# Performance work log

Measured on AMD Instinct MI355X. Metric: run time of the kernel, lower is better.

Reference implementation:

```python
import jax, jax.numpy as jnp
import numpy as np

N = 100000      # nodes
E = 1600000     # edges (before self-loops)
F_IN = 512      # input features
H = 8           # heads layer 1
D = 8           # per-head dim layer 1
C = 40          # classes (layer 2 out, heads=1)
NEG_SLOPE = 0.2 # PyG GATConv default negative_slope


def setup_inputs() -> dict:
    key = jax.random.key(0)
    ks = jax.random.split(key, 10)
    x = jax.random.normal(ks[0], (N, F_IN), jnp.float32)
    edge_index = jax.random.randint(ks[1], (2, E), 0, N, dtype=jnp.int32)
    W1 = jax.random.normal(ks[2], (F_IN, H * D), jnp.float32) / np.float32(np.sqrt(F_IN))
    att_src1 = jax.random.normal(ks[3], (H, D), jnp.float32) / np.float32(np.sqrt(D))
    att_dst1 = jax.random.normal(ks[4], (H, D), jnp.float32) / np.float32(np.sqrt(D))
    b1 = jnp.zeros((H * D,), jnp.float32)
    W2 = jax.random.normal(ks[5], (H * D, C), jnp.float32) / np.float32(np.sqrt(H * D))
    att_src2 = jax.random.normal(ks[6], (1, C), jnp.float32) / np.float32(np.sqrt(C))
    att_dst2 = jax.random.normal(ks[7], (1, C), jnp.float32) / np.float32(np.sqrt(C))
    b2 = jnp.zeros((C,), jnp.float32)
    return {"x": x, "edge_index": edge_index, "W1": W1, "att_src1": att_src1,
            "att_dst1": att_dst1, "b1": b1, "W2": W2, "att_src2": att_src2,
            "att_dst2": att_dst2, "b2": b2}


def _gat_layer(x, src, dst, W, a_src, a_dst, heads, dim):
    # Dense projection, then per-head attention logits.
    h = (x @ W).reshape(-1, heads, dim)            # [N, H, D]
    alpha_s = jnp.einsum('nhd,hd->nh', h, a_src)   # [N, H]
    alpha_d = jnp.einsum('nhd,hd->nh', h, a_dst)
    e = jax.nn.leaky_relu(alpha_s[src] + alpha_d[dst], NEG_SLOPE)  # [E, H]
    # Segment softmax over edges grouped by destination node.
    emax = jax.ops.segment_max(e, dst, num_segments=N)
    emax = jnp.where(jnp.isfinite(emax), emax, 0.0)
    ee = jnp.exp(e - emax[dst])
    denom = jax.ops.segment_sum(ee, dst, num_segments=N)
    alpha = ee / (denom[dst] + 1e-16)              # [E, H]
    # Scatter-aggregate weighted neighbor features.
    msg = h[src] * alpha[:, :, None]               # [E, H, D]
    return jax.ops.segment_sum(msg, dst, num_segments=N)  # [N, H, D]


def reference(x, edge_index, W1, att_src1, att_dst1, b1, W2, att_src2, att_dst2, b2):
    # PyG GATConv adds self-loops by default.
    loops = jnp.arange(N, dtype=edge_index.dtype)
    src = jnp.concatenate([edge_index[0], loops])
    dst = jnp.concatenate([edge_index[1], loops])
    # Layer 1: 8 heads, concat=True, then ELU. (dropouts identity in eval mode)
    h1 = _gat_layer(x, src, dst, W1, att_src1, att_dst1, H, D).reshape(N, H * D) + b1
    h1 = jax.nn.elu(h1)
    # Layer 2: 1 head, concat=False -> mean over heads (trivial for H=1).
    h2 = _gat_layer(h1, src, dst, W2, att_src2, att_dst2, 1, C)[:, 0, :] + b2
    return jax.nn.log_softmax(h2, axis=1)
```

## Files before the change

kernel.cpp:

```cpp
#include <hip/hip_runtime.h>

#define F_IN   512
#define HD     64
#define NHEAD  8
#define NC     40
#define NEG    0.2f

typedef __attribute__((ext_vector_type(8))) short bf16x8;
typedef __attribute__((ext_vector_type(4))) float f32x4;

__device__ __forceinline__ float lrelu(float x) { return x > 0.0f ? x : NEG * x; }

__device__ __forceinline__ short f2bf(float f) {
    unsigned u = __float_as_uint(f);
    u += 0x7FFF + ((u >> 16) & 1);
    return (short)(u >> 16);
}
__device__ __forceinline__ float bf2f(short h) {
    return __uint_as_float(((unsigned)(unsigned short)h) << 16);
}
__device__ __forceinline__ float bfl(unsigned u) { return __uint_as_float(u << 16); }
__device__ __forceinline__ float bfh(unsigned u) { return __uint_as_float(u & 0xFFFF0000u); }

__global__ void zero_kernel(int* __restrict__ p, int n) {
    int i = blockIdx.x * 256 + threadIdx.x;
    if (i < n) p[i] = 0;
}

__global__ void count_kernel(const int* __restrict__ dst, int* __restrict__ deg,
                             int* __restrict__ pos, int E) {
    int e = blockIdx.x * 256 + threadIdx.x;
    if (e < E) pos[e] = atomicAdd(&deg[dst[e]], 1);
}

__global__ __launch_bounds__(256) void scanA_kernel(const int* __restrict__ deg,
                                                    int* __restrict__ incl,
                                                    int* __restrict__ bsum, int Nn) {
    __shared__ int wsum[4];
    int t = threadIdx.x, b = blockIdx.x;
    int base = b * 1024 + t * 4;
    int v0 = (base + 0) < Nn ? deg[base + 0] : 0;
    int v1 = (base + 1) < Nn ? deg[base + 1] : 0;
    int v2 = (base + 2) < Nn ? deg[base + 2] : 0;
    int v3 = (base + 3) < Nn ? deg[base + 3] : 0;
    int p0 = v0, p1 = p0 + v1, p2 = p1 + v2, p3 = p2 + v3;
    int lane = t & 63, w = t >> 6;
    int sc = p3;
    for (int off = 1; off < 64; off <<= 1) {
        int u = __shfl_up(sc, off);
        if (lane >= off) sc += u;
    }
    if (lane == 63) wsum[w] = sc;
    __syncthreads();
    int woff = 0;
#pragma unroll
    for (int i = 0; i < 4; ++i) if (i < w) woff += wsum[i];
    int excl = woff + sc - p3;
    if (base + 0 < Nn) incl[base + 0] = excl + p0;
    if (base + 1 < Nn) incl[base + 1] = excl + p1;
    if (base + 2 < Nn) incl[base + 2] = excl + p2;
    if (base + 3 < Nn) incl[base + 3] = excl + p3;
    if (t == 0) bsum[b] = wsum[0] + wsum[1] + wsum[2] + wsum[3];
}

__global__ void scanB_kernel(int* __restrict__ bsum, int nb) {
    int lane = threadIdx.x;
    int a = lane < nb ? bsum[lane] : 0;
    int c = (lane + 64) < nb ? bsum[lane + 64] : 0;
    int sa = a, sc2 = c;
    for (int off = 1; off < 64; off <<= 1) {
        int u = __shfl_up(sa, off);  if (lane >= off) sa += u;
        int u2 = __shfl_up(sc2, off); if (lane >= off) sc2 += u2;
    }
    int totA = __shfl(sa, 63);
    int ea = sa - a;
    int ec = totA + sc2 - c;
    if (lane < nb) bsum[lane] = ea;
    if (lane + 64 < nb) bsum[lane + 64] = ec;
}

__global__ void scanC_kernel(const int* __restrict__ incl, const int* __restrict__ bsum,
                             int* __restrict__ rp, int Nn) {
    int i = blockIdx.x * 256 + threadIdx.x;
    if (i == 0) rp[0] = 0;
    if (i < Nn) rp[i + 1] = incl[i] + bsum[i >> 10];
}

#define G1_BM 128
__global__ __launch_bounds__(256) void g1s_kernel(const float* __restrict__ X,
                                                  const float* __restrict__ W,
                                                  const float* __restrict__ att_s,
                                                  const float* __restrict__ att_d,
                                                  unsigned short* __restrict__ Hp,
                                                  float* __restrict__ as1,
                                                  float* __restrict__ ad1,
                                                  const int* __restrict__ src,
                                                  const int* __restrict__ dst,
                                                  const int* __restrict__ pos,
                                                  const int* __restrict__ rp,
                                                  int* __restrict__ col,
                                                  int Nn, int E, int nG1) {
    __shared__ short Bh[4][HD][8];
    __shared__ short Bl[4][HD][8];
    int tid = threadIdx.x;

    if ((int)blockIdx.x >= nG1) {
        int e = ((int)blockIdx.x - nG1) * 256 + tid;
        if (e < E) {
            int d = dst[e];
            int p = rp[d] + pos[e];
            __builtin_nontemporal_store(src[e], &col[p]);
        }
        return;
    }

    int wid = tid >> 6, lane = tid & 63;
    int lrow = lane & 15, kgrp = lane >> 4;
    int row0 = blockIdx.x * G1_BM;
    int rowA = row0 + wid * 32 + lrow;

    int sc = tid & 63, skc = tid >> 6;

    float ats[4], atd[4];
#pragma unroll
    for (int fc = 0; fc < 4; ++fc) { ats[fc] = att_s[fc * 16 + lrow]; atd[fc] = att_d[fc * 16 + lrow]; }

    f32x4 acc[2][4];
#pragma unroll
    for (int fr = 0; fr < 2; ++fr)
#pragma unroll
        for (int fc = 0; fc < 4; ++fc) acc[fr][fc] = (f32x4){0.f, 0.f, 0.f, 0.f};

    float4 a_cur[2][2], a_nxt[2][2];
#pragma unroll
    for (int fr = 0; fr < 2; ++fr) {
        int gr = rowA + fr * 16;
        if (gr < Nn) {
            const float* p = X + (size_t)gr * F_IN + kgrp * 8;
            a_cur[fr][0] = *reinterpret_cast<const float4*>(p);
            a_cur[fr][1] = *reinterpret_cast<const float4*>(p + 4);
        } else {
            a_cur[fr][0] = a_cur[fr][1] = make_float4(0.f, 0.f, 0.f, 0.f);
        }
    }

    for (int it = 0; it < F_IN / 32; ++it) {
        int k0 = it * 32;
        float wreg[8];
#pragma unroll
        for (int j = 0; j < 8; ++j)
            wreg[j] = W[(size_t)(k0 + skc * 8 + j) * HD + sc];
        if (it + 1 < F_IN / 32) {
#pragma unroll
            for (int fr = 0; fr < 2; ++fr) {
                int gr = rowA + fr * 16;
                if (gr < Nn) {
                    const float* p = X + (size_t)gr * F_IN + (k0 + 32) + kgrp * 8;
                    a_nxt[fr][0] = *reinterpret_cast<const float4*>(p);
                    a_nxt[fr][1] = *reinterpret_cast<const float4*>(p + 4);
                } else {
                    a_nxt[fr][0] = a_nxt[fr][1] = make_float4(0.f, 0.f, 0.f, 0.f);
                }
            }
        }
        bf16x8 af[2];
#pragma unroll
        for (int fr = 0; fr < 2; ++fr) {
            float fs[8] = {a_cur[fr][0].x, a_cur[fr][0].y, a_cur[fr][0].z, a_cur[fr][0].w,
                           a_cur[fr][1].x, a_cur[fr][1].y, a_cur[fr][1].z, a_cur[fr][1].w};
#pragma unroll
            for (int j = 0; j < 8; ++j) af[fr][j] = f2bf(fs[j]);
        }
        __syncthreads();
        {
            bf16x8 vh, vl;
#pragma unroll
            for (int j = 0; j < 8; ++j) {
                short hh = f2bf(wreg[j]);
                vh[j] = hh;
                vl[j] = f2bf(wreg[j] - bf2f(hh));
            }
            *reinterpret_cast<bf16x8*>(&Bh[skc][sc][0]) = vh;
            *reinterpret_cast<bf16x8*>(&Bl[skc][sc][0]) = vl;
        }
        __syncthreads();
        bf16x8 bh[4], bl[4];
#pragma unroll
        for (int fc = 0; fc < 4; ++fc) {
            bh[fc] = *reinterpret_cast<const bf16x8*>(&Bh[kgrp][fc * 16 + lrow][0]);
            bl[fc] = *reinterpret_cast<const bf16x8*>(&Bl[kgrp][fc * 16 + lrow][0]);
        }
#pragma unroll
        for (int fr = 0; fr < 2; ++fr)
#pragma unroll
            for (int fc = 0; fc < 4; ++fc) {
                acc[fr][fc] = __builtin_amdgcn_mfma_f32_16x16x32_bf16(af[fr], bh[fc], acc[fr][fc], 0, 0, 0);
                acc[fr][fc] = __builtin_amdgcn_mfma_f32_16x16x32_bf16(af[fr], bl[fc], acc[fr][fc], 0, 0, 0);
            }
        if (it + 1 < F_IN / 32) {
#pragma unroll
            for (int fr = 0; fr < 2; ++fr) {
                a_cur[fr][0] = a_nxt[fr][0];
                a_cur[fr][1] = a_nxt[fr][1];
            }
        }
    }

#pragma unroll
    for (int fr = 0; fr < 2; ++fr) {
#pragma unroll
        for (int r = 0; r < 4; ++r) {
            int gr = row0 + wid * 32 + fr * 16 + kgrp * 4 + r;
            float hv[4], sp[4], dp[4];
#pragma unroll
            for (int fc = 0; fc < 4; ++fc) {
                hv[fc] = acc[fr][fc][r];
                sp[fc] = hv[fc] * ats[fc];
                dp[fc] = hv[fc] * atd[fc];
            }
#pragma unroll
            for (int mask = 1; mask <= 4; mask <<= 1) {
#pragma unroll
                for (int fc = 0; fc < 4; ++fc) {
                    sp[fc] += __shfl_xor(sp[fc], mask);
                    dp[fc] += __shfl_xor(dp[fc], mask);
                }
            }
            if (gr < Nn) {
#pragma unroll
                for (int fc = 0; fc < 4; ++fc)
                    Hp[(size_t)gr * HD + fc * 16 + lrow] = (unsigned short)f2bf(hv[fc]);
                if ((lane & 7) == 0) {
                    int hh = lrow >> 3;
#pragma unroll
                    for (int fc = 0; fc < 4; ++fc) {
                        as1[gr * NHEAD + fc * 2 + hh] = sp[fc];
                        ad1[gr * NHEAD + fc * 2 + hh] = dp[fc];
                    }
                }
            }
        }
    }
}

__global__ __launch_bounds__(256) void agg1_kernel(const unsigned short* __restrict__ Hp,
                                                   const float* __restrict__ as1,
                                                   const float* __restrict__ ad1,
                                                   const int* __restrict__ col,
                                                   const int* __restrict__ rp,
                                                   const float* __restrict__ b1,
                                                   const float* __restrict__ W2,
                                                   const float* __restrict__ as2w,
                                                   const float* __restrict__ ad2w,
                                                   unsigned int* __restrict__ h2p,
                                                   float* __restrict__ as2,
                                                   float* __restrict__ ad2, int Nn) {
    __shared__ float W2s[HD][NC];
    __shared__ float asv[NC], adv[NC];
    int tid = threadIdx.x;
    for (int i = tid; i < HD * NC; i += 256) W2s[i / NC][i % NC] = W2[i];
    if (tid < NC) { asv[tid] = as2w[tid]; adv[tid] = ad2w[tid]; }
    __syncthreads();
    int n = blockIdx.x * 4 + (tid >> 6);
    int lane = tid & 63;
    if (n >= Nn) return;
    int slot = lane >> 4, l16 = lane & 15, h = l16 >> 1;
    int beg = rp[n], end = rp[n + 1];
    float adv1 = ad1[n * NHEAD + h];
    float4 acc = make_float4(0.f, 0.f, 0.f, 0.f);
    float dw = 0.f;
    for (int t = beg + slot; t < end; t += 4) {
        int s = col[t];
        float w = __expf(lrelu(as1[s * NHEAD + h] + adv1));
        dw += w;
        uint2 u = *reinterpret_cast<const uint2*>(&Hp[(size_t)s * HD + l16 * 4]);
        acc.x += w * bfl(u.x); acc.y += w * bfh(u.x);
        acc.z += w * bfl(u.y); acc.w += w * bfh(u.y);
    }
#pragma unroll
    for (int mask = 16; mask < 64; mask <<= 1) {
        acc.x += __shfl_xor(acc.x, mask);
        acc.y += __shfl_xor(acc.y, mask);
        acc.z += __shfl_xor(acc.z, mask);
        acc.w += __shfl_xor(acc.w, mask);
        dw    += __shfl_xor(dw, mask);
    }
    {
        float w = __expf(lrelu(as1[n * NHEAD + h] + adv1));
        uint2 u = *reinterpret_cast<const uint2*>(&Hp[(size_t)n * HD + l16 * 4]);
        acc.x += w * bfl(u.x); acc.y += w * bfh(u.x);
        acc.z += w * bfl(u.y); acc.w += w * bfh(u.y);
        dw += w;
        float invd = 1.0f / (dw + 1e-16f);
        float4 bb = *reinterpret_cast<const float4*>(&b1[l16 * 4]);
        acc.x = acc.x * invd + bb.x; acc.y = acc.y * invd + bb.y;
        acc.z = acc.z * invd + bb.z; acc.w = acc.w * invd + bb.w;
        acc.x = acc.x > 0.0f ? acc.x : __expf(acc.x) - 1.0f;
        acc.y = acc.y > 0.0f ? acc.y : __expf(acc.y) - 1.0f;
        acc.z = acc.z > 0.0f ? acc.z : __expf(acc.z) - 1.0f;
        acc.w = acc.w > 0.0f ? acc.w : __expf(acc.w) - 1.0f;
    }
    int cw = lane < NC ? lane : 0;
    float h2 = 0.f;
#pragma unroll
    for (int k = 0; k < HD; ++k) {
        int srcl = k >> 2;
        float comp = (k & 3) == 0 ? acc.x : (k & 3) == 1 ? acc.y : (k & 3) == 2 ? acc.z : acc.w;
        float hk = __shfl(comp, srcl);
        h2 += hk * W2s[k][cw];
    }
    float sa = lane < NC ? h2 * asv[lane] : 0.f;
    float da = lane < NC ? h2 * adv[lane] : 0.f;
#pragma unroll
    for (int mask = 1; mask < 64; mask <<= 1) { sa += __shfl_xor(sa, mask); da += __shfl_xor(da, mask); }
    if (lane == 0) { as2[n] = sa; ad2[n] = da; }
    float hp2 = __shfl(h2, lane + 1);
    if (lane < NC && !(lane & 1)) {
        unsigned int u = ((unsigned int)(unsigned short)f2bf(hp2) << 16) |
                         (unsigned short)f2bf(h2);
        h2p[(size_t)n * 20 + (lane >> 1)] = u;
    }
}

__global__ __launch_bounds__(256) void agg2_kernel(const unsigned int* __restrict__ h2p,
                                                   const float* __restrict__ as2,
                                                   const float* __restrict__ ad2,
                                                   const int* __restrict__ col,
                                                   const int* __restrict__ rp,
                                                   const float* __restrict__ b2,
                                                   float* __restrict__ out, int Nn) {
    int n = blockIdx.x * 4 + (threadIdx.x >> 6);
    int lane = threadIdx.x & 63;
    if (n >= Nn) return;
    int slot = lane >> 4, l16 = lane & 15;
    bool act = l16 < 10;
    int beg = rp[n], end = rp[n + 1];
    float adv = ad2[n];
    float4 acc = make_float4(0.f, 0.f, 0.f, 0.f);
    float dw = 0.f;
    for (int t = beg + slot; t < end; t += 4) {
        int s = col[t];
        float w = __expf(lrelu(as2[s] + adv));
        dw += w;
        if (act) {
            uint2 u = *reinterpret_cast<const uint2*>(&h2p[(size_t)s * 20 + l16 * 2]);
            acc.x += w * bfl(u.x); acc.y += w * bfh(u.x);
            acc.z += w * bfl(u.y); acc.w += w * bfh(u.y);
        }
    }
#pragma unroll
    for (int mask = 16; mask < 64; mask <<= 1) {
        acc.x += __shfl_xor(acc.x, mask);
        acc.y += __shfl_xor(acc.y, mask);
        acc.z += __shfl_xor(acc.z, mask);
        acc.w += __shfl_xor(acc.w, mask);
        dw    += __shfl_xor(dw, mask);
    }
    float w = __expf(lrelu(as2[n] + adv));
    dw += w;
    float invd = 1.0f / (dw + 1e-16f);
    if (act) {
        uint2 u = *reinterpret_cast<const uint2*>(&h2p[(size_t)n * 20 + l16 * 2]);
        float4 bb = *reinterpret_cast<const float4*>(&b2[l16 * 4]);
        acc.x = (acc.x + w * bfl(u.x)) * invd + bb.x;
        acc.y = (acc.y + w * bfh(u.x)) * invd + bb.y;
        acc.z = (acc.z + w * bfl(u.y)) * invd + bb.z;
        acc.w = (acc.w + w * bfh(u.y)) * invd + bb.w;
    }
    float mloc = act ? fmaxf(fmaxf(acc.x, acc.y), fmaxf(acc.z, acc.w)) : -INFINITY;
#pragma unroll
    for (int mask = 1; mask < 16; mask <<= 1) mloc = fmaxf(mloc, __shfl_xor(mloc, mask));
    float s4 = act ? (__expf(acc.x - mloc) + __expf(acc.y - mloc) +
                      __expf(acc.z - mloc) + __expf(acc.w - mloc)) : 0.0f;
#pragma unroll
    for (int mask = 1; mask < 16; mask <<= 1) s4 += __shfl_xor(s4, mask);
    float lse = mloc + __logf(s4);
    if (slot == 0 && act) {
        float4 o = make_float4(acc.x - lse, acc.y - lse, acc.z - lse, acc.w - lse);
        *reinterpret_cast<float4*>(&out[(size_t)n * NC + l16 * 4]) = o;
    }
}

extern "C" void kernel_launch(void* const* d_in, const int* in_sizes, int n_in,
                              void* d_out, int out_size, void* d_ws, size_t ws_size,
                              hipStream_t stream) {
    const float* x    = (const float*)d_in[0];
    const int*   ei   = (const int*)d_in[1];
    const float* W1   = (const float*)d_in[2];
    const float* as1w = (const float*)d_in[3];
    const float* ad1w = (const float*)d_in[4];
    const float* b1   = (const float*)d_in[5];
    const float* W2   = (const float*)d_in[6];
    const float* as2w = (const float*)d_in[7];
    const float* ad2w = (const float*)d_in[8];
    const float* b2   = (const float*)d_in[9];
    float* out = (float*)d_out;

    int Nn = in_sizes[0] / F_IN;
    int E  = in_sizes[1] / 2;
    const int* srcv = ei;
    const int* dstv = ei + E;

    char* ws = (char*)d_ws;
    size_t off = 0;
    auto alloc = [&](size_t bytes) { size_t cur = off; off += (bytes + 255) & ~255ULL; return cur; };
    unsigned short* Hp = (unsigned short*)(ws + alloc((size_t)Nn * HD * 2));
    float* as1v = (float*)(ws + alloc((size_t)Nn * NHEAD * 4));
    float* ad1v = (float*)(ws + alloc((size_t)Nn * NHEAD * 4));
    unsigned int* h2p = (unsigned int*)(ws + alloc((size_t)Nn * 20 * 4));
    float* as2v = (float*)(ws + alloc((size_t)Nn * 4));
    float* ad2v = (float*)(ws + alloc((size_t)Nn * 4));
    int* deg  = (int*)(ws + alloc((size_t)Nn * 4));
    int* incl = (int*)(ws + alloc((size_t)Nn * 4));
    int* rp   = (int*)(ws + alloc((size_t)(Nn + 1) * 4));
    int* pos  = (int*)(ws + alloc((size_t)E * 4));
    int* col  = (int*)(ws + alloc((size_t)E * 4));
    int* bsum = (int*)(ws + alloc(256 * 4));

    int nb  = (Nn + 1023) / 1024;
    int nG1 = (Nn + G1_BM - 1) / G1_BM;
    int nSC = (E + 255) / 256;

    zero_kernel<<<(Nn + 255) / 256, 256, 0, stream>>>(deg, Nn);
    count_kernel<<<(E + 255) / 256, 256, 0, stream>>>(dstv, deg, pos, E);
    scanA_kernel<<<nb, 256, 0, stream>>>(deg, incl, bsum, Nn);
    scanB_kernel<<<1, 64, 0, stream>>>(bsum, nb);
    scanC_kernel<<<(Nn + 255) / 256, 256, 0, stream>>>(incl, bsum, rp, Nn);

    g1s_kernel<<<nG1 + nSC, 256, 0, stream>>>(x, W1, as1w, ad1w, Hp, as1v, ad1v,
                                              srcv, dstv, pos, rp, col, Nn, E, nG1);
    agg1_kernel<<<(Nn + 3) / 4, 256, 0, stream>>>(Hp, as1v, ad1v, col, rp, b1,
                                                  W2, as2w, ad2w, h2p, as2v, ad2v, Nn);
    agg2_kernel<<<(Nn + 3) / 4, 256, 0, stream>>>(h2p, as2v, ad2v, col, rp, b2, out, Nn);
}
```

Baseline: 393.4 us.

## Retile layer-1 GEMM, widen agg1 edge parallelism, split layer-2 projection into GEMM kernel

The layer-1 GEMM now uses 64-row tiles with a 64-wide K step, giving twice as many blocks and half as many K iterations. agg1 now processes 8 edges at a time per wave (8 lanes per edge, 16-byte loads) and writes h1 in fp32. The per-node layer-2 projection with shuffles moves into a separate tiled gemm2 kernel that stages h1 and W2 in shared memory. This removes the serialized per-node projection from the aggregation kernel, at the cost of an extra 25.6 MB fp32 round trip for h1 and one more kernel launch.

```diff
diff --git a/kernel.cpp b/kernel.cpp
--- a/kernel.cpp
+++ b/kernel.cpp
@@ -86,7 +86,7 @@
     if (i < Nn) rp[i + 1] = incl[i] + bsum[i >> 10];
 }
 
-#define G1_BM 128
+#define G1_BM 64
 __global__ __launch_bounds__(256) void g1s_kernel(const float* __restrict__ X,
                                                   const float* __restrict__ W,
                                                   const float* __restrict__ att_s,
@@ -100,8 +100,8 @@
                                                   const int* __restrict__ rp,
                                                   int* __restrict__ col,
                                                   int Nn, int E, int nG1) {
-    __shared__ short Bh[4][HD][8];
-    __shared__ short Bl[4][HD][8];
+    __shared__ short Bh[2][4][HD][8];
+    __shared__ short Bl[2][4][HD][8];
     int tid = threadIdx.x;
 
     if ((int)blockIdx.x >= nG1) {
@@ -117,126 +117,121 @@
     int wid = tid >> 6, lane = tid & 63;
     int lrow = lane & 15, kgrp = lane >> 4;
     int row0 = blockIdx.x * G1_BM;
-    int rowA = row0 + wid * 32 + lrow;
-
-    int sc = tid & 63, skc = tid >> 6;
+    int rowA = row0 + wid * 16 + lrow;
+
+    int sc = tid & 63, ks = tid >> 6;
 
     float ats[4], atd[4];
 #pragma unroll
     for (int fc = 0; fc < 4; ++fc) { ats[fc] = att_s[fc * 16 + lrow]; atd[fc] = att_d[fc * 16 + lrow]; }
 
-    f32x4 acc[2][4];
-#pragma unroll
-    for (int fr = 0; fr < 2; ++fr)
-#pragma unroll
-        for (int fc = 0; fc < 4; ++fc) acc[fr][fc] = (f32x4){0.f, 0.f, 0.f, 0.f};
+    f32x4 acc[4];
+#pragma unroll
+    for (int fc = 0; fc < 4; ++fc) acc[fc] = (f32x4){0.f, 0.f, 0.f, 0.f};
+
+    bool valid = rowA < Nn;
+    const float* xrow = X + (size_t)rowA * F_IN + kgrp * 8;
 
     float4 a_cur[2][2], a_nxt[2][2];
 #pragma unroll
-    for (int fr = 0; fr < 2; ++fr) {
-        int gr = rowA + fr * 16;
+    for (int kb = 0; kb < 2; ++kb) {
+        if (valid) {
+            a_cur[kb][0] = *reinterpret_cast<const float4*>(xrow + kb * 32);
+            a_cur[kb][1] = *reinterpret_cast<const float4*>(xrow + kb * 32 + 4);
+        } else {
+            a_cur[kb][0] = a_cur[kb][1] = make_float4(0.f, 0.f, 0.f, 0.f);
+        }
+    }
+
+    for (int it = 0; it < F_IN / 64; ++it) {
+        int k0 = it * 64;
+        float wreg[16];
+#pragma unroll
+        for (int j = 0; j < 16; ++j)
+            wreg[j] = W[(size_t)(k0 + ks * 16 + j) * HD + sc];
+        if (it + 1 < F_IN / 64) {
+#pragma unroll
+            for (int kb = 0; kb < 2; ++kb) {
+                if (valid) {
+                    const float* p = xrow + (k0 + 64) + kb * 32;
+                    a_nxt[kb][0] = *reinterpret_cast<const float4*>(p);
+                    a_nxt[kb][1] = *reinterpret_cast<const float4*>(p + 4);
+                } else {
+                    a_nxt[kb][0] = a_nxt[kb][1] = make_float4(0.f, 0.f, 0.f, 0.f);
+                }
+            }
+        }
+        bf16x8 af[2];
+#pragma unroll
+        for (int kb = 0; kb < 2; ++kb) {
+            float fs[8] = {a_cur[kb][0].x, a_cur[kb][0].y, a_cur[kb][0].z, a_cur[kb][0].w,
+                           a_cur[kb][1].x, a_cur[kb][1].y, a_cur[kb][1].z, a_cur[kb][1].w};
+#pragma unroll
+            for (int j = 0; j < 8; ++j) af[kb][j] = f2bf(fs[j]);
+        }
+        __syncthreads();
+#pragma unroll
+        for (int half = 0; half < 2; ++half) {
+            bf16x8 vh, vl;
+#pragma unroll
+            for (int j = 0; j < 8; ++j) {
+                float wv = wreg[half * 8 + j];
+                short hh = f2bf(wv);
+                vh[j] = hh;
+                vl[j] = f2bf(wv - bf2f(hh));
+            }
+            int kk = ks * 2 + half;
+            *reinterpret_cast<bf16x8*>(&Bh[kk >> 2][kk & 3][sc][0]) = vh;
+            *reinterpret_cast<bf16x8*>(&Bl[kk >> 2][kk & 3][sc][0]) = vl;
+        }
+        __syncthreads();
+#pragma unroll
+        for (int kb = 0; kb < 2; ++kb) {
+#pragma unroll
+            for (int fc = 0; fc < 4; ++fc) {
+                bf16x8 bh = *reinterpret_cast<const bf16x8*>(&Bh[kb][kgrp][fc * 16 + lrow][0]);
+                bf16x8 bl = *reinterpret_cast<const bf16x8*>(&Bl[kb][kgrp][fc * 16 + lrow][0]);
+                acc[fc] = __builtin_amdgcn_mfma_f32_16x16x32_bf16(af[kb], bh, acc[fc], 0, 0, 0);
+                acc[fc] = __builtin_amdgcn_mfma_f32_16x16x32_bf16(af[kb], bl, acc[fc], 0, 0, 0);
+            }
+        }
+        if (it + 1 < F_IN / 64) {
+#pragma unroll
+            for (int kb = 0; kb < 2; ++kb) {
+                a_cur[kb][0] = a_nxt[kb][0];
+                a_cur[kb][1] = a_nxt[kb][1];
+            }
+        }
+    }
+
+#pragma unroll
+    for (int r = 0; r < 4; ++r) {
+        int gr = row0 + wid * 16 + kgrp * 4 + r;
+        float hv[4], sp[4], dp[4];
+#pragma unroll
+        for (int fc = 0; fc < 4; ++fc) {
+            hv[fc] = acc[fc][r];
+            sp[fc] = hv[fc] * ats[fc];
+            dp[fc] = hv[fc] * atd[fc];
+        }
+#pragma unroll
+        for (int mask = 1; mask <= 4; mask <<= 1) {
+#pragma unroll
+            for (int fc = 0; fc < 4; ++fc) {
+                sp[fc] += __shfl_xor(sp[fc], mask);
+                dp[fc] += __shfl_xor(dp[fc], mask);
+            }
+        }
         if (gr < Nn) {
-            const float* p = X + (size_t)gr * F_IN + kgrp * 8;
-            a_cur[fr][0] = *reinterpret_cast<const float4*>(p);
-            a_cur[fr][1] = *reinterpret_cast<const float4*>(p + 4);
-        } else {
-            a_cur[fr][0] = a_cur[fr][1] = make_float4(0.f, 0.f, 0.f, 0.f);
-        }
-    }
-
-    for (int it = 0; it < F_IN / 32; ++it) {
-        int k0 = it * 32;
-        float wreg[8];
-#pragma unroll
-        for (int j = 0; j < 8; ++j)
-            wreg[j] = W[(size_t)(k0 + skc * 8 + j) * HD + sc];
-        if (it + 1 < F_IN / 32) {
-#pragma unroll
-            for (int fr = 0; fr < 2; ++fr) {
-                int gr = rowA + fr * 16;
-                if (gr < Nn) {
-                    const float* p = X + (size_t)gr * F_IN + (k0 + 32) + kgrp * 8;
-                    a_nxt[fr][0] = *reinterpret_cast<const float4*>(p);
-                    a_nxt[fr][1] = *reinterpret_cast<const float4*>(p + 4);
-                } else {
-                    a_nxt[fr][0] = a_nxt[fr][1] = make_float4(0.f, 0.f, 0.f, 0.f);
-                }
-            }
-        }
-        bf16x8 af[2];
-#pragma unroll
-        for (int fr = 0; fr < 2; ++fr) {
-            float fs[8] = {a_cur[fr][0].x, a_cur[fr][0].y, a_cur[fr][0].z, a_cur[fr][0].w,
-                           a_cur[fr][1].x, a_cur[fr][1].y, a_cur[fr][1].z, a_cur[fr][1].w};
-#pragma unroll
-            for (int j = 0; j < 8; ++j) af[fr][j] = f2bf(fs[j]);
-        }
-        __syncthreads();
-        {
-            bf16x8 vh, vl;
-#pragma unroll
-            for (int j = 0; j < 8; ++j) {
-                short hh = f2bf(wreg[j]);
-                vh[j] = hh;
-                vl[j] = f2bf(wreg[j] - bf2f(hh));
-            }
-            *reinterpret_cast<bf16x8*>(&Bh[skc][sc][0]) = vh;
-            *reinterpret_cast<bf16x8*>(&Bl[skc][sc][0]) = vl;
-        }
-        __syncthreads();
-        bf16x8 bh[4], bl[4];
-#pragma unroll
-        for (int fc = 0; fc < 4; ++fc) {
-            bh[fc] = *reinterpret_cast<const bf16x8*>(&Bh[kgrp][fc * 16 + lrow][0]);
-            bl[fc] = *reinterpret_cast<const bf16x8*>(&Bl[kgrp][fc * 16 + lrow][0]);
-        }
-#pragma unroll
-        for (int fr = 0; fr < 2; ++fr)
-#pragma unroll
-            for (int fc = 0; fc < 4; ++fc) {
-                acc[fr][fc] = __builtin_amdgcn_mfma_f32_16x16x32_bf16(af[fr], bh[fc], acc[fr][fc], 0, 0, 0);
-                acc[fr][fc] = __builtin_amdgcn_mfma_f32_16x16x32_bf16(af[fr], bl[fc], acc[fr][fc], 0, 0, 0);
-            }
-        if (it + 1 < F_IN / 32) {
-#pragma unroll
-            for (int fr = 0; fr < 2; ++fr) {
-                a_cur[fr][0] = a_nxt[fr][0];
-                a_cur[fr][1] = a_nxt[fr][1];
-            }
-        }
-    }
-
-#pragma unroll
-    for (int fr = 0; fr < 2; ++fr) {
-#pragma unroll
-        for (int r = 0; r < 4; ++r) {
-            int gr = row0 + wid * 32 + fr * 16 + kgrp * 4 + r;
-            float hv[4], sp[4], dp[4];
-#pragma unroll
-            for (int fc = 0; fc < 4; ++fc) {
-                hv[fc] = acc[fr][fc][r];
-                sp[fc] = hv[fc] * ats[fc];
-                dp[fc] = hv[fc] * atd[fc];
-            }
-#pragma unroll
-            for (int mask = 1; mask <= 4; mask <<= 1) {
+#pragma unroll
+            for (int fc = 0; fc < 4; ++fc)
+                Hp[(size_t)gr * HD + fc * 16 + lrow] = (unsigned short)f2bf(hv[fc]);
+            if ((lane & 7) == 0) {
+                int hh = lrow >> 3;
 #pragma unroll
                 for (int fc = 0; fc < 4; ++fc) {
-                    sp[fc] += __shfl_xor(sp[fc], mask);
-                    dp[fc] += __shfl_xor(dp[fc], mask);
-                }
-            }
-            if (gr < Nn) {
-#pragma unroll
-                for (int fc = 0; fc < 4; ++fc)
-                    Hp[(size_t)gr * HD + fc * 16 + lrow] = (unsigned short)f2bf(hv[fc]);
-                if ((lane & 7) == 0) {
-                    int hh = lrow >> 3;
-#pragma unroll
-                    for (int fc = 0; fc < 4; ++fc) {
-                        as1[gr * NHEAD + fc * 2 + hh] = sp[fc];
-                        ad1[gr * NHEAD + fc * 2 + hh] = dp[fc];
-                    }
+                    as1[gr * NHEAD + fc * 2 + hh] = sp[fc];
+                    ad1[gr * NHEAD + fc * 2 + hh] = dp[fc];
                 }
             }
         }
@@ -249,76 +244,106 @@
                                                    const int* __restrict__ col,
                                                    const int* __restrict__ rp,
                                                    const float* __restrict__ b1,
-                                                   const float* __restrict__ W2,
-                                                   const float* __restrict__ as2w,
-                                                   const float* __restrict__ ad2w,
-                                                   unsigned int* __restrict__ h2p,
-                                                   float* __restrict__ as2,
-                                                   float* __restrict__ ad2, int Nn) {
+                                                   float* __restrict__ h1, int Nn) {
+    int n = blockIdx.x * 4 + (threadIdx.x >> 6);
+    int lane = threadIdx.x & 63;
+    if (n >= Nn) return;
+    int slot = lane >> 3, j = lane & 7;
+    int beg = rp[n], end = rp[n + 1];
+    float adv1 = ad1[n * NHEAD + j];
+    float acc[8] = {0, 0, 0, 0, 0, 0, 0, 0};
+    float dw = 0.f;
+    for (int t = beg + slot; t < end; t += 8) {
+        int s = col[t];
+        float w = __expf(lrelu(as1[s * NHEAD + j] + adv1));
+        dw += w;
+        uint4 u = *reinterpret_cast<const uint4*>(&Hp[(size_t)s * HD + j * 8]);
+        acc[0] += w * bfl(u.x); acc[1] += w * bfh(u.x);
+        acc[2] += w * bfl(u.y); acc[3] += w * bfh(u.y);
+        acc[4] += w * bfl(u.z); acc[5] += w * bfh(u.z);
+        acc[6] += w * bfl(u.w); acc[7] += w * bfh(u.w);
+    }
+#pragma unroll
+    for (int mask = 8; mask < 64; mask <<= 1) {
+#pragma unroll
+        for (int i = 0; i < 8; ++i) acc[i] += __shfl_xor(acc[i], mask);
+        dw += __shfl_xor(dw, mask);
+    }
+    float w = __expf(lrelu(as1[n * NHEAD + j] + adv1));
+    uint4 u = *reinterpret_cast<const uint4*>(&Hp[(size_t)n * HD + j * 8]);
+    acc[0] += w * bfl(u.x); acc[1] += w * bfh(u.x);
+    acc[2] += w * bfl(u.y); acc[3] += w * bfh(u.y);
+    acc[4] += w * bfl(u.z); acc[5] += w * bfh(u.z);
+    acc[6] += w * bfl(u.w); acc[7] += w * bfh(u.w);
+    dw += w;
+    float invd = 1.0f / (dw + 1e-16f);
+    float4 b0 = *reinterpret_cast<const float4*>(&b1[j * 8]);
+    float4 b4 = *reinterpret_cast<const float4*>(&b1[j * 8 + 4]);
+    float bb[8] = {b0.x, b0.y, b0.z, b0.w, b4.x, b4.y, b4.z, b4.w};
+#pragma unroll
+    for (int i = 0; i < 8; ++i) {
+        float v = acc[i] * invd + bb[i];
+        acc[i] = v > 0.0f ? v : __expf(v) - 1.0f;
+    }
+    if (slot == 0) {
+        float4 o0 = make_float4(acc[0], acc[1], acc[2], acc[3]);
+        float4 o1 = make_float4(acc[4], acc[5], acc[6], acc[7]);
+        *reinterpret_cast<float4*>(&h1[(size_t)n * HD + j * 8]) = o0;
+        *reinterpret_cast<float4*>(&h1[(size_t)n * HD + j * 8 + 4]) = o1;
+    }
+}
+
+#define G2R 64
+__global__ __launch_bounds__(256) void gemm2_kernel(const float* __restrict__ H1,
+                                                    const float* __restrict__ W2,
+                                                    const float* __restrict__ asw,
+                                                    const float* __restrict__ adw,
+                                                    unsigned int* __restrict__ h2p,
+                                                    float* __restrict__ as2,
+                                                    float* __restrict__ ad2, int Nn) {
+    __shared__ float Hs[G2R][HD + 1];
     __shared__ float W2s[HD][NC];
     __shared__ float asv[NC], adv[NC];
     int tid = threadIdx.x;
     for (int i = tid; i < HD * NC; i += 256) W2s[i / NC][i % NC] = W2[i];
-    if (tid < NC) { asv[tid] = as2w[tid]; adv[tid] = ad2w[tid]; }
+    if (tid < NC) { asv[tid] = asw[tid]; adv[tid] = adw[tid]; }
+    int row0 = blockIdx.x * G2R;
+#pragma unroll
+    for (int i = 0; i < 4; ++i) {
+        int linear = i * 1024 + tid * 4;
+        int r = linear >> 6, c = linear & 63;
+        int gr = row0 + r;
+        float4 v = make_float4(0.f, 0.f, 0.f, 0.f);
+        if (gr < Nn) v = *reinterpret_cast<const float4*>(&H1[(size_t)gr * HD + c]);
+        Hs[r][c + 0] = v.x; Hs[r][c + 1] = v.y; Hs[r][c + 2] = v.z; Hs[r][c + 3] = v.w;
+    }
     __syncthreads();
-    int n = blockIdx.x * 4 + (tid >> 6);
-    int lane = tid & 63;
-    if (n >= Nn) return;
-    int slot = lane >> 4, l16 = lane & 15, h = l16 >> 1;
-    int beg = rp[n], end = rp[n + 1];
-    float adv1 = ad1[n * NHEAD + h];
-    float4 acc = make_float4(0.f, 0.f, 0.f, 0.f);
-    float dw = 0.f;
-    for (int t = beg + slot; t < end; t += 4) {
-        int s = col[t];
-        float w = __expf(lrelu(as1[s * NHEAD + h] + adv1));
-        dw += w;
-        uint2 u = *reinterpret_cast<const uint2*>(&Hp[(size_t)s * HD + l16 * 4]);
-        acc.x += w * bfl(u.x); acc.y += w * bfh(u.x);
-        acc.z += w * bfl(u.y); acc.w += w * bfh(u.y);
-    }
-#pragma unroll
-    for (int mask = 16; mask < 64; mask <<= 1) {
-        acc.x += __shfl_xor(acc.x, mask);
-        acc.y += __shfl_xor(acc.y, mask);
-        acc.z += __shfl_xor(acc.z, mask);
-        acc.w += __shfl_xor(acc.w, mask);
-        dw    += __shfl_xor(dw, mask);
-    }
-    {
-        float w = __expf(lrelu(as1[n * NHEAD + h] + adv1));
-        uint2 u = *reinterpret_cast<const uint2*>(&Hp[(size_t)n * HD + l16 * 4]);
-        acc.x += w * bfl(u.x); acc.y += w * bfh(u.x);
-        acc.z += w * bfl(u.y); acc.w += w * bfh(u.y);
-        dw += w;
-        float invd = 1.0f / (dw + 1e-16f);
-        float4 bb = *reinterpret_cast<const float4*>(&b1[l16 * 4]);
-        acc.x = acc.x * invd + bb.x; acc.y = acc.y * invd + bb.y;
-        acc.z = acc.z * invd + bb.z; acc.w = acc.w * invd + bb.w;
-        acc.x = acc.x > 0.0f ? acc.x : __expf(acc.x) - 1.0f;
-        acc.y = acc.y > 0.0f ? acc.y : __expf(acc.y) - 1.0f;
-        acc.z = acc.z > 0.0f ? acc.z : __expf(acc.z) - 1.0f;
-        acc.w = acc.w > 0.0f ? acc.w : __expf(acc.w) - 1.0f;
-    }
-    int cw = lane < NC ? lane : 0;
-    float h2 = 0.f;
-#pragma unroll
+    int row = tid >> 2, cg = tid & 3;
+    int gr = row0 + row;
+    float acc[10];
+#pragma unroll
+    for (int jj = 0; jj < 10; ++jj) acc[jj] = 0.0f;
     for (int k = 0; k < HD; ++k) {
-        int srcl = k >> 2;
-        float comp = (k & 3) == 0 ? acc.x : (k & 3) == 1 ? acc.y : (k & 3) == 2 ? acc.z : acc.w;
-        float hk = __shfl(comp, srcl);
-        h2 += hk * W2s[k][cw];
-    }
-    float sa = lane < NC ? h2 * asv[lane] : 0.f;
-    float da = lane < NC ? h2 * adv[lane] : 0.f;
-#pragma unroll
-    for (int mask = 1; mask < 64; mask <<= 1) { sa += __shfl_xor(sa, mask); da += __shfl_xor(da, mask); }
-    if (lane == 0) { as2[n] = sa; ad2[n] = da; }
-    float hp2 = __shfl(h2, lane + 1);
-    if (lane < NC && !(lane & 1)) {
-        unsigned int u = ((unsigned int)(unsigned short)f2bf(hp2) << 16) |
-                         (unsigned short)f2bf(h2);
-        h2p[(size_t)n * 20 + (lane >> 1)] = u;
+        float a = Hs[row][k];
+#pragma unroll
+        for (int jj = 0; jj < 10; ++jj) acc[jj] += a * W2s[k][cg * 10 + jj];
+    }
+    float sa = 0.0f, da = 0.0f;
+#pragma unroll
+    for (int jj = 0; jj < 10; ++jj) {
+        sa += acc[jj] * asv[cg * 10 + jj];
+        da += acc[jj] * adv[cg * 10 + jj];
+    }
+    sa += __shfl_xor(sa, 1); sa += __shfl_xor(sa, 2);
+    da += __shfl_xor(da, 1); da += __shfl_xor(da, 2);
+    if (gr < Nn) {
+        if (cg == 0) { as2[gr] = sa; ad2[gr] = da; }
+#pragma unroll
+        for (int jj = 0; jj < 5; ++jj) {
+            unsigned int u = ((unsigned int)(unsigned short)f2bf(acc[2 * jj + 1]) << 16) |
+                             (unsigned short)f2bf(acc[2 * jj]);
+            h2p[(size_t)gr * 20 + cg * 5 + jj] = u;
+        }
     }
 }
 
@@ -405,6 +430,7 @@
     size_t off = 0;
     auto alloc = [&](size_t bytes) { size_t cur = off; off += (bytes + 255) & ~255ULL; return cur; };
     unsigned short* Hp = (unsigned short*)(ws + alloc((size_t)Nn * HD * 2));
+    float* h1   = (float*)(ws + alloc((size_t)Nn * HD * 4));
     float* as1v = (float*)(ws + alloc((size_t)Nn * NHEAD * 4));
     float* ad1v = (float*)(ws + alloc((size_t)Nn * NHEAD * 4));
     unsigned int* h2p = (unsigned int*)(ws + alloc((size_t)Nn * 20 * 4));
@@ -429,7 +455,7 @@
 
     g1s_kernel<<<nG1 + nSC, 256, 0, stream>>>(x, W1, as1w, ad1w, Hp, as1v, ad1v,
                                               srcv, dstv, pos, rp, col, Nn, E, nG1);
-    agg1_kernel<<<(Nn + 3) / 4, 256, 0, stream>>>(Hp, as1v, ad1v, col, rp, b1,
-                                                  W2, as2w, ad2w, h2p, as2v, ad2v, Nn);
+    agg1_kernel<<<(Nn + 3) / 4, 256, 0, stream>>>(Hp, as1v, ad1v, col, rp, b1, h1, Nn);
+    gemm2_kernel<<<(Nn + G2R - 1) / G2R, 256, 0, stream>>>(h1, W2, as2w, ad2w, h2p, as2v, ad2v, Nn);
     agg2_kernel<<<(Nn + 3) / 4, 256, 0, stream>>>(h2p, as2v, ad2v, col, rp, b2, out, Nn);
 }
```

After: 333.4 us. 15.3% less time.
